# Optimization experiments

Hardware: AMD Instinct MI355X
Metric: run time of the kernel (lower is better)

## Reference

```python
import jax, jax.numpy as jnp
import numpy as np
from jax import lax

N = 4194304  # batch of FP16 values, each encoded as 16 spike bits

# MSB-first bit weights / shift amounts for the [S,E4..E0,M9..M0] layout
_POW = np.array([1 << (15 - i) for i in range(16)], dtype=np.int32)
_SHIFTS = np.array([15 - i for i in range(16)], dtype=np.int32)


def _pack(bits):
    """[..., 16] {0,1} float bits (MSB first) -> float16 scalar per row."""
    b = jnp.round(bits).astype(jnp.int32)
    u = jnp.sum(b * _POW, axis=-1).astype(jnp.uint16)
    return lax.bitcast_convert_type(u, jnp.float16)


def _unpack(f):
    """float16 [...] -> [..., 16] {0,1} float32 bits (MSB first)."""
    u = lax.bitcast_convert_type(f, jnp.uint16).astype(jnp.int32)
    return ((u[..., None] >> _SHIFTS) & 1).astype(jnp.float32)


def _sample_bits(key, n):
    bits = jax.random.bernoulli(key, 0.5, (n, 16)).astype(jnp.float32)
    # avoid exponent == 31 (Inf/NaN encodings) so outputs are well-defined finite fp16
    all_ones = jnp.prod(bits[:, 1:6], axis=-1, keepdims=True)
    return bits.at[:, 5:6].set(bits[:, 5:6] * (1.0 - all_ones))


def setup_inputs() -> dict:
    key = jax.random.key(0)
    ka, kb = jax.random.split(key)
    return {"A": _sample_bits(ka, N), "B": _sample_bits(kb, N)}


def reference(A, B):
    # The SNN gate network implements an IEEE-754 FP16 adder (round-to-nearest-even,
    # subnormal support, overflow/underflow handling) over bit-encoded operands.
    # fp16 add computed via fp32 is bit-exact here (24 >= 2*11+2, Figueroa's theorem),
    # which is what XLA does for float16 on CPU.
    s = _pack(A) + _pack(B)
    return _unpack(s)
```

## Files before the change

kernel.cpp:

```cpp
#include <hip/hip_runtime.h>
#include <hip/hip_fp16.h>


__global__ __launch_bounds__(256) void spike_fp16_add_kernel(
    const float4* __restrict__ A, const float4* __restrict__ B,
    float4* __restrict__ O, int nf4)
{
    const int lane = threadIdx.x & 63;
    const int waveBase = ((blockIdx.x * blockDim.x + threadIdx.x) >> 6) * 256;
    const int q = lane & 3;
    const int sh = 12 - 4 * q;

    #pragma unroll
    for (int k = 0; k < 4; ++k) {
        const int f4 = waveBase + k * 64 + lane;
        if (f4 >= nf4) return;

        float4 a = A[f4];
        float4 b = B[f4];

        uint32_t na = ((uint32_t)a.x << 3) | ((uint32_t)a.y << 2) |
                      ((uint32_t)a.z << 1) |  (uint32_t)a.w;
        uint32_t nb = ((uint32_t)b.x << 3) | ((uint32_t)b.y << 2) |
                      ((uint32_t)b.z << 1) |  (uint32_t)b.w;

        uint32_t ua = na << sh;
        uint32_t ub = nb << sh;

        ua |= (uint32_t)__shfl_xor((int)ua, 1);
        ua |= (uint32_t)__shfl_xor((int)ua, 2);
        ub |= (uint32_t)__shfl_xor((int)ub, 1);
        ub |= (uint32_t)__shfl_xor((int)ub, 2);

        float fa = __half2float(__ushort_as_half((unsigned short)ua));
        float fb = __half2float(__ushort_as_half((unsigned short)ub));
        uint32_t us = (uint32_t)__half_as_ushort(__float2half_rn(fa + fb));

        uint32_t ns = (us >> sh) & 0xFu;
        float4 o;
        o.x = (float)((ns >> 3) & 1u);
        o.y = (float)((ns >> 2) & 1u);
        o.z = (float)((ns >> 1) & 1u);
        o.w = (float)( ns       & 1u);

        O[f4] = o;
    }
}

extern "C" void kernel_launch(void* const* d_in, const int* in_sizes, int n_in,
                              void* d_out, int out_size, void* d_ws, size_t ws_size,
                              hipStream_t stream) {
    const float4* A = (const float4*)d_in[0];
    const float4* B = (const float4*)d_in[1];
    float4* O = (float4*)d_out;

    int nf4 = in_sizes[0] / 4;
    int block = 256;
    int threads = nf4 / 4;
    int grid = (threads + block - 1) / block;
    spike_fp16_add_kernel<<<grid, block, 0, stream>>>(A, B, O, nf4);
}
```

Baseline: 577.3 us.

## Batch loads up front, use DPP swizzles and nontemporal stores

Splits the work into a fast path for full waves and a guarded tail path. The fast path issues all eight 16-byte loads before computing, to raise memory-level parallelism. It also extracts bits directly from the float bit patterns instead of converting float to int, packs both operands into one word so a single pair of DPP quad swizzles replaces four shuffles, and writes output with nontemporal stores. The kernel is memory bound, so the gain rests mainly on the load batching and streaming stores, at the cost of more registers per thread.

```diff
diff --git a/kernel.cpp b/kernel.cpp
--- a/kernel.cpp
+++ b/kernel.cpp
@@ -2,61 +2,92 @@
 #include <hip/hip_fp16.h>
 
 
+typedef float fx4 __attribute__((ext_vector_type(4)));
+
 __global__ __launch_bounds__(256) void spike_fp16_add_kernel(
-    const float4* __restrict__ A, const float4* __restrict__ B,
+    const uint4* __restrict__ A, const uint4* __restrict__ B,
     float4* __restrict__ O, int nf4)
 {
     const int lane = threadIdx.x & 63;
     const int waveBase = ((blockIdx.x * blockDim.x + threadIdx.x) >> 6) * 256;
-    const int q = lane & 3;
+    const int q  = lane & 3;
     const int sh = 12 - 4 * q;
 
-    #pragma unroll
-    for (int k = 0; k < 4; ++k) {
-        const int f4 = waveBase + k * 64 + lane;
-        if (f4 >= nf4) return;
+    if (waveBase + 256 <= nf4) {
+        uint4 a[4], b[4];
+        #pragma unroll
+        for (int k = 0; k < 4; ++k) {
+            a[k] = A[waveBase + k * 64 + lane];
+            b[k] = B[waveBase + k * 64 + lane];
+        }
 
-        float4 a = A[f4];
-        float4 b = B[f4];
+        #pragma unroll
+        for (int k = 0; k < 4; ++k) {
+            uint32_t na = ((a[k].x >> 20) & 8u) | ((a[k].y >> 21) & 4u) |
+                          ((a[k].z >> 22) & 2u) | ((a[k].w >> 23) & 1u);
+            uint32_t nb = ((b[k].x >> 20) & 8u) | ((b[k].y >> 21) & 4u) |
+                          ((b[k].z >> 22) & 2u) | ((b[k].w >> 23) & 1u);
 
-        uint32_t na = ((uint32_t)a.x << 3) | ((uint32_t)a.y << 2) |
-                      ((uint32_t)a.z << 1) |  (uint32_t)a.w;
-        uint32_t nb = ((uint32_t)b.x << 3) | ((uint32_t)b.y << 2) |
-                      ((uint32_t)b.z << 1) |  (uint32_t)b.w;
+            uint32_t w = (na << sh) | (nb << (sh + 16));
 
-        uint32_t ua = na << sh;
-        uint32_t ub = nb << sh;
+            w |= (uint32_t)__builtin_amdgcn_mov_dpp((int)w, 0xB1, 0xF, 0xF, true);
+            w |= (uint32_t)__builtin_amdgcn_mov_dpp((int)w, 0x4E, 0xF, 0xF, true);
 
-        ua |= (uint32_t)__shfl_xor((int)ua, 1);
-        ua |= (uint32_t)__shfl_xor((int)ua, 2);
-        ub |= (uint32_t)__shfl_xor((int)ub, 1);
-        ub |= (uint32_t)__shfl_xor((int)ub, 2);
+            float fa = __half2float(__ushort_as_half((unsigned short)(w & 0xFFFFu)));
+            float fb = __half2float(__ushort_as_half((unsigned short)(w >> 16)));
+            uint32_t us = (uint32_t)__half_as_ushort(__float2half_rn(fa + fb));
 
-        float fa = __half2float(__ushort_as_half((unsigned short)ua));
-        float fb = __half2float(__ushort_as_half((unsigned short)ub));
-        uint32_t us = (uint32_t)__half_as_ushort(__float2half_rn(fa + fb));
+            uint32_t ns = (us >> sh) & 0xFu;
+            fx4 o;
+            o.x = (float)((ns >> 3) & 1u);
+            o.y = (float)((ns >> 2) & 1u);
+            o.z = (float)((ns >> 1) & 1u);
+            o.w = (float)( ns       & 1u);
 
-        uint32_t ns = (us >> sh) & 0xFu;
-        float4 o;
-        o.x = (float)((ns >> 3) & 1u);
-        o.y = (float)((ns >> 2) & 1u);
-        o.z = (float)((ns >> 1) & 1u);
-        o.w = (float)( ns       & 1u);
+            __builtin_nontemporal_store(
+                o, (fx4*)&O[waveBase + k * 64 + lane]);
+        }
+    } else {
+        #pragma unroll
+        for (int k = 0; k < 4; ++k) {
+            const int f4 = waveBase + k * 64 + lane;
+            if (f4 >= nf4) continue;
 
-        O[f4] = o;
+            uint4 a = A[f4];
+            uint4 b = B[f4];
+            uint32_t na = ((a.x >> 20) & 8u) | ((a.y >> 21) & 4u) |
+                          ((a.z >> 22) & 2u) | ((a.w >> 23) & 1u);
+            uint32_t nb = ((b.x >> 20) & 8u) | ((b.y >> 21) & 4u) |
+                          ((b.z >> 22) & 2u) | ((b.w >> 23) & 1u);
+            uint32_t w = (na << sh) | (nb << (sh + 16));
+            w |= (uint32_t)__shfl_xor((int)w, 1);
+            w |= (uint32_t)__shfl_xor((int)w, 2);
+
+            float fa = __half2float(__ushort_as_half((unsigned short)(w & 0xFFFFu)));
+            float fb = __half2float(__ushort_as_half((unsigned short)(w >> 16)));
+            uint32_t us = (uint32_t)__half_as_ushort(__float2half_rn(fa + fb));
+
+            uint32_t ns = (us >> sh) & 0xFu;
+            float4 o;
+            o.x = (float)((ns >> 3) & 1u);
+            o.y = (float)((ns >> 2) & 1u);
+            o.z = (float)((ns >> 1) & 1u);
+            o.w = (float)( ns       & 1u);
+            O[f4] = o;
+        }
     }
 }
 
 extern "C" void kernel_launch(void* const* d_in, const int* in_sizes, int n_in,
                               void* d_out, int out_size, void* d_ws, size_t ws_size,
                               hipStream_t stream) {
-    const float4* A = (const float4*)d_in[0];
-    const float4* B = (const float4*)d_in[1];
+    const uint4* A = (const uint4*)d_in[0];
+    const uint4* B = (const uint4*)d_in[1];
     float4* O = (float4*)d_out;
 
     int nf4 = in_sizes[0] / 4;
     int block = 256;
-    int threads = nf4 / 4;
+    int threads = (nf4 + 3) / 4;
     int grid = (threads + block - 1) / block;
     spike_fp16_add_kernel<<<grid, block, 0, stream>>>(A, B, O, nf4);
 }
```

New measurement: 584.9 us. Within noise of the previous version (+1.3%).
